# Optimization experiments

Measured on AMD Instinct MI355X. Metric: run time of the kernel, lower is better.

Reference implementation:

```python
import jax, jax.numpy as jnp
import numpy as np

BATCH = 1024
M = 64      # N_v measurements
N = 8192    # N_theta unknowns
STEPS = 3   # N_admm_steps
EPS_DIV = 1e-12


def setup_inputs() -> dict:
    key = jax.random.key(0)
    k = jax.random.split(key, 4)
    return {
        "r_n": jax.random.normal(k[0], (BATCH, 2, N), jnp.float32),
        "y": jax.random.normal(k[1], (BATCH, 2, M), jnp.float32),
        "u_in": jax.random.normal(k[2], (BATCH, 2, M), jnp.float32),
        "A": jax.random.normal(k[3], (2, M, N), jnp.float32) / np.sqrt(N).astype(np.float32),
        "log_rho": jnp.zeros((), jnp.float32),                 # rho = 1.0
        "log_epsilon": jnp.asarray(np.log(0.01), jnp.float32), # epsilon = 0.01
    }


def _cmm(Ar, Ai, v):
    # complex matmul A @ v : v [b,2,N] -> [b,2,M]
    vr, vi = v[:, 0], v[:, 1]
    return jnp.stack([vr @ Ar.T - vi @ Ai.T, vi @ Ar.T + vr @ Ai.T], axis=1)


def _chm(Ar, Ai, v):
    # complex conj-transpose matmul A^H @ v : v [b,2,M] -> [b,2,N]
    vr, vi = v[:, 0], v[:, 1]
    return jnp.stack([vr @ Ar + vi @ Ai, vi @ Ar - vr @ Ai], axis=1)


def reference(r_n, y, u_in, A, log_rho, log_epsilon):
    rho = jnp.exp(log_rho)
    epsilon = jnp.exp(log_epsilon)
    Ar, Ai = A[0], A[1]  # [M, N]

    # SMW system matrix: S = (1/rho) I + A A^H, written as real 2Mx2M block matrix.
    # It is constant across ADMM steps (rho fixed within a forward pass).
    I_M = jnp.eye(M, dtype=A.dtype)
    S_r = I_M / (rho + EPS_DIV) + Ar @ Ar.T + Ai @ Ai.T
    S_i = Ai @ Ar.T - Ar @ Ai.T
    S_block = jnp.block([[S_r, -S_i], [S_i, S_r]])  # [2M, 2M]

    x, z, u = r_n, y, u_in
    for _ in range(STEPS):
        # x-update via SMW: x = b - A^H (S^{-1} A b), b = r_n + rho A^H (z - u)
        b = r_n + rho * _chm(Ar, Ai, z - u)          # [b,2,N]
        Ab = _cmm(Ar, Ai, b)                          # [b,2,M]
        R = jnp.concatenate([Ab[:, 0], Ab[:, 1]], axis=1)  # [b,2M]
        sol = jnp.linalg.solve(S_block, R.T)          # [2M, b]
        T = jnp.stack([sol[:M].T, sol[M:].T], axis=1)  # [b,2,M]
        x = b - _chm(Ar, Ai, T)                       # [b,2,N]
        # enforce_real: zero imaginary part; enforce_positivity: clamp real part
        x = jnp.stack([jnp.maximum(x[:, 0], 0.0), jnp.zeros_like(x[:, 0])], axis=1)
        # z-update: project residual onto complex L2 ball of radius epsilon
        Ax = _cmm(Ar, Ai, x)                          # [b,2,M]
        v = Ax + u - y
        nrm = jnp.sqrt(jnp.sum(v * v, axis=(1, 2), keepdims=True))
        z = y + v * jnp.minimum(1.0, epsilon / (nrm + EPS_DIV))
        # dual update
        u = u + Ax - z
    return x, u
```

## Files before the change

### kernel.cpp

```cpp
#include <hip/hip_runtime.h>

#define B_ 1024
#define M_ 64
#define N_ 8192
#define NSG 16
#define NS3 8

typedef __attribute__((ext_vector_type(8))) short bf16x8;
typedef __attribute__((ext_vector_type(4))) float f32x4;

__device__ inline unsigned short f2b(float f) {
    union { float f; unsigned u; } v; v.f = f;
    unsigned r = v.u + 0x7FFFu + ((v.u >> 16) & 1u);
    return (unsigned short)(r >> 16);
}
__device__ inline unsigned rne2(float lo, float hi) {
    union { float f; unsigned u; } a, b; a.f = lo; b.f = hi;
    unsigned x = (a.u + 0x7FFFu + ((a.u >> 16) & 1u)) >> 16;
    unsigned y = (b.u + 0x7FFFu + ((b.u >> 16) & 1u)) >> 16;
    return x | (y << 16);
}
__device__ inline float b2f(unsigned short s) {
    union { unsigned u; float f; } v; v.u = ((unsigned)s) << 16; return v.f;
}
__device__ inline float rl(float v, int l) {
    return __builtin_bit_cast(float, __builtin_amdgcn_readlane(__builtin_bit_cast(int, v), l));
}

__global__ __launch_bounds__(256) void k_cvt(const float* src, unsigned short* dst) {
    size_t i = ((size_t)blockIdx.x * 256 + threadIdx.x) * 8;
    float4 f0 = *(const float4*)(src + i);
    float4 f1 = *(const float4*)(src + i + 4);
    union { bf16x8 v; unsigned u[4]; } r;
    r.u[0] = rne2(f0.x, f0.y); r.u[1] = rne2(f0.z, f0.w);
    r.u[2] = rne2(f1.x, f1.y); r.u[3] = rne2(f1.z, f1.w);
    *(bf16x8*)(dst + i) = r.v;
}

__global__ __launch_bounds__(256) void k_prep(const float* A, unsigned short* Abf,
                                              unsigned short* WgT, unsigned short* ATb) {
    __shared__ float tile[128][65];
    int n0 = blockIdx.x * 64;
    int t = threadIdx.x;
    int nl = t % 64, r0 = t / 64;
#pragma unroll
    for (int it = 0; it < 32; ++it) {
        int row = r0 + it * 4;
        tile[row][nl] = A[(size_t)row * N_ + n0 + nl];
    }
    __syncthreads();
#pragma unroll
    for (int it = 0; it < 32; ++it) {
        int row = r0 + it * 4;
        float v = tile[row][nl];
        unsigned short bv = f2b(v);
        Abf[(size_t)row * N_ + n0 + nl] = bv;
        if (row < 64) {
            WgT[(size_t)row * 16384 + n0 + nl] = bv;
            WgT[(size_t)(64 + row) * 16384 + 8192 + n0 + nl] = bv;
        } else {
            int m = row - 64;
            WgT[(size_t)m * 16384 + 8192 + n0 + nl] = f2b(-v);
            WgT[(size_t)(64 + m) * 16384 + n0 + nl] = bv;
        }
    }
    int o = t % 128, nn0 = t / 128;
#pragma unroll
    for (int it = 0; it < 32; ++it) {
        int nn = nn0 + it * 2;
        ATb[(size_t)(n0 + nn) * 128 + o] = f2b(tile[o][nn]);
    }
}

__global__ __launch_bounds__(256) void k_Sbuild(const float* A, const float* lr,
                                                float* S, float* AAHT) {
    __shared__ float redS[8];
    int bid = blockIdx.x;
    int i = 0, rem = bid;
    while (rem >= 64 - i) { rem -= 64 - i; ++i; }
    int j = i + rem;
    int t = threadIdx.x;
    const float* Ar = A;
    const float* Ai = A + (size_t)M_ * N_;
    const float* ari = Ar + (size_t)i * N_;
    const float* aii = Ai + (size_t)i * N_;
    const float* arj = Ar + (size_t)j * N_;
    const float* aij = Ai + (size_t)j * N_;
    float aR = 0.f, aI = 0.f;
#pragma unroll
    for (int it = 0; it < 8; ++it) {
        int n = it * 1024 + t * 4;
        float4 xr = *(const float4*)(ari + n);
        float4 xi = *(const float4*)(aii + n);
        float4 br = *(const float4*)(arj + n);
        float4 bi = *(const float4*)(aij + n);
        aR += xr.x * br.x + xi.x * bi.x + xr.y * br.y + xi.y * bi.y
            + xr.z * br.z + xi.z * bi.z + xr.w * br.w + xi.w * bi.w;
        aI += xi.x * br.x - xr.x * bi.x + xi.y * br.y - xr.y * bi.y
            + xi.z * br.z - xr.z * bi.z + xi.w * br.w - xr.w * bi.w;
    }
    for (int off = 32; off > 0; off >>= 1) {
        aR += __shfl_down(aR, off, 64);
        aI += __shfl_down(aI, off, 64);
    }
    int lane = t & 63, w = t >> 6;
    if (lane == 0) { redS[w * 2] = aR; redS[w * 2 + 1] = aI; }
    __syncthreads();
    if (t == 0) {
        float R = redS[0] + redS[2] + redS[4] + redS[6];
        float I = redS[1] + redS[3] + redS[5] + redS[7];
        float inv_rho = 1.0f / (expf(lr[0]) + 1e-12f);
        float diag = (i == j) ? inv_rho : 0.f;
        S[((size_t)i * 64 + j) * 2 + 0] = R + diag;
        S[((size_t)i * 64 + j) * 2 + 1] = I;
        AAHT[((size_t)j * 64 + i) * 2 + 0] = R;
        AAHT[((size_t)j * 64 + i) * 2 + 1] = I;
        if (i != j) {
            S[((size_t)j * 64 + i) * 2 + 0] = R;
            S[((size_t)j * 64 + i) * 2 + 1] = -I;
            AAHT[((size_t)i * 64 + j) * 2 + 0] = R;
            AAHT[((size_t)i * 64 + j) * 2 + 1] = -I;
        }
    }
}

__global__ __launch_bounds__(256, 2) void k_Ginv(const unsigned short* rnb,
                                                 const unsigned short* WgT,
                                                 float* Gpart,
                                                 const float* S, float* Wt) {
    int t = threadIdx.x;
    int lane = t & 63;
    if (blockIdx.x == 0) {
        __shared__ float2 fvs[2][64];
        int g = t >> 6;
        float mx0,my0,mx1,my1,mx2,my2,mx3,my3,mx4,my4,mx5,my5,mx6,my6,mx7,my7;
        float mx8,my8,mx9,my9,mx10,my10,mx11,my11,mx12,my12,mx13,my13,mx14,my14,mx15,my15;
#define GJ_INIT(J) { int c = 4 * (J) + g;                                    \
    float2 v = ((const float2*)S)[(size_t)lane * 64 + c];                    \
    mx##J = v.x; my##J = v.y; }
        GJ_INIT(0) GJ_INIT(1) GJ_INIT(2) GJ_INIT(3) GJ_INIT(4) GJ_INIT(5) GJ_INIT(6) GJ_INIT(7)
        GJ_INIT(8) GJ_INIT(9) GJ_INIT(10) GJ_INIT(11) GJ_INIT(12) GJ_INIT(13) GJ_INIT(14) GJ_INIT(15)
#undef GJ_INIT
        for (int k = 0; k < 64; ++k) {
            const int par = k & 1;
            if (g == (k & 3)) {
                switch (k >> 2) {
                    case 0:  fvs[par][lane] = make_float2(mx0,  my0);  break;
                    case 1:  fvs[par][lane] = make_float2(mx1,  my1);  break;
                    case 2:  fvs[par][lane] = make_float2(mx2,  my2);  break;
                    case 3:  fvs[par][lane] = make_float2(mx3,  my3);  break;
                    case 4:  fvs[par][lane] = make_float2(mx4,  my4);  break;
                    case 5:  fvs[par][lane] = make_float2(mx5,  my5);  break;
                    case 6:  fvs[par][lane] = make_float2(mx6,  my6);  break;
                    case 7:  fvs[par][lane] = make_float2(mx7,  my7);  break;
                    case 8:  fvs[par][lane] = make_float2(mx8,  my8);  break;
                    case 9:  fvs[par][lane] = make_float2(mx9,  my9);  break;
                    case 10: fvs[par][lane] = make_float2(mx10, my10); break;
                    case 11: fvs[par][lane] = make_float2(mx11, my11); break;
                    case 12: fvs[par][lane] = make_float2(mx12, my12); break;
                    case 13: fvs[par][lane] = make_float2(mx13, my13); break;
                    case 14: fvs[par][lane] = make_float2(mx14, my14); break;
                    default: fvs[par][lane] = make_float2(mx15, my15); break;
                }
            }
            __syncthreads();
            float2 f = fvs[par][lane];
            float2 p = fvs[par][k];
            float d = p.x * p.x + p.y * p.y;
            float id = 1.0f / d;
            float pix = p.x * id, piy = -p.y * id;
            bool isk = (lane == k);
            float a   = isk ? 0.f : 1.f;
            float fpx = isk ? -pix : (f.x * pix - f.y * piy);
            float fpy = isk ? -piy : (f.x * piy + f.y * pix);
#define GJ_UP(J) { if (4 * (J) + g == k) { mx##J = -fpx; my##J = -fpy; }     \
    else {                                                                   \
    float sx = rl(mx##J, k), sy = rl(my##J, k);                              \
    float nx = a * mx##J - (fpx * sx - fpy * sy);                            \
    float ny = a * my##J - (fpx * sy + fpy * sx);                            \
    mx##J = nx; my##J = ny; } }
            GJ_UP(0) GJ_UP(1) GJ_UP(2) GJ_UP(3) GJ_UP(4) GJ_UP(5) GJ_UP(6) GJ_UP(7)
            GJ_UP(8) GJ_UP(9) GJ_UP(10) GJ_UP(11) GJ_UP(12) GJ_UP(13) GJ_UP(14) GJ_UP(15)
#undef GJ_UP
        }
#define GJ_OUT(J) { int c = 4 * (J) + g;                                     \
    ((float2*)Wt)[(size_t)c * 64 + lane] = make_float2(mx##J, my##J); }
        GJ_OUT(0) GJ_OUT(1) GJ_OUT(2) GJ_OUT(3) GJ_OUT(4) GJ_OUT(5) GJ_OUT(6) GJ_OUT(7)
        GJ_OUT(8) GJ_OUT(9) GJ_OUT(10) GJ_OUT(11) GJ_OUT(12) GJ_OUT(13) GJ_OUT(14) GJ_OUT(15)
#undef GJ_OUT
        return;
    }
    int bx = blockIdx.x - 1;
    int w = t >> 6;
    int l15 = lane & 15;
    int q8 = (lane >> 4) * 8;
    int split = bx & 15;
    int b0 = (bx >> 4) * 16;
    int k0 = split * 1024;
    f32x4 a00 = {}, a01 = {};
    const unsigned short* x0 = rnb + (size_t)(b0 + l15) * 16384 + k0 + q8;
    const unsigned short* w0 = WgT + (size_t)(w * 32 + l15) * 16384 + k0 + q8;
    const unsigned short* w1 = w0 + (size_t)16 * 16384;
#pragma unroll 8
    for (int ks = 0; ks < 32; ++ks) {
        int kk = ks * 32;
        bf16x8 af0 = *(const bf16x8*)(x0 + kk);
        bf16x8 bf0 = *(const bf16x8*)(w0 + kk);
        bf16x8 bf1 = *(const bf16x8*)(w1 + kk);
        a00 = __builtin_amdgcn_mfma_f32_16x16x32_bf16(af0, bf0, a00, 0, 0, 0);
        a01 = __builtin_amdgcn_mfma_f32_16x16x32_bf16(af0, bf1, a01, 0, 0, 0);
    }
    int row = (lane >> 4) * 4;
    size_t base = (size_t)split * (B_ * 128);
    float* g = Gpart + base + (size_t)(b0 + row) * 128 + w * 32 + l15;
#pragma unroll
    for (int r = 0; r < 4; ++r) {
        g[(size_t)r * 128] = a00[r];
        g[(size_t)r * 128 + 16] = a01[r];
    }
}

__global__ __launch_bounds__(256) void k_small12(const float* Gpart, const float* AAHT,
                                                 const float* Wt, const float* zin,
                                                 const float* uin, const float* lr,
                                                 unsigned short* qb) {
    __shared__ float2 AbS[4][64];
    int t = threadIdx.x;
    int m = t & 63;
    int w = __builtin_amdgcn_readfirstlane(t >> 6);
    int b = blockIdx.x * 4 + w;
    float rho = expf(lr[0]);
    float abR = 0.f, abI = 0.f;
    for (int k = 0; k < 64; ++k) {
        float wr = zin[(b * 2 + 0) * 64 + k] - uin[(b * 2 + 0) * 64 + k];
        float wi = zin[(b * 2 + 1) * 64 + k] - uin[(b * 2 + 1) * 64 + k];
        float2 h = *(const float2*)(AAHT + ((size_t)k * 64 + m) * 2);
        abR += wr * h.x - wi * h.y;
        abI += wi * h.x + wr * h.y;
    }
    float gR = 0.f, gI = 0.f;
#pragma unroll
    for (int s = 0; s < NSG; ++s) {
        gR += Gpart[(size_t)s * 131072 + (size_t)b * 128 + m];
        gI += Gpart[(size_t)s * 131072 + (size_t)b * 128 + 64 + m];
    }
    abR = gR + rho * abR;
    abI = gI + rho * abI;
    AbS[w][m] = make_float2(abR, abI);
    __syncthreads();
    float tR = 0.f, tI = 0.f;
    for (int k = 0; k < 64; ++k) {
        float2 Wv = *(const float2*)(Wt + ((size_t)k * 64 + m) * 2);
        float2 ab = AbS[w][k];
        tR += ab.x * Wv.x - ab.y * Wv.y;
        tI += ab.y * Wv.x + ab.x * Wv.y;
    }
    float wr_m = zin[(b * 2 + 0) * 64 + m] - uin[(b * 2 + 0) * 64 + m];
    float wi_m = zin[(b * 2 + 1) * 64 + m] - uin[(b * 2 + 1) * 64 + m];
    qb[(size_t)b * 128 + m] = f2b(rho * wr_m - tR);
    qb[(size_t)b * 128 + 64 + m] = f2b(rho * wi_m - tI);
}

__global__ __launch_bounds__(256, 3) void k_H23(const unsigned short* qb, const unsigned short* ATb,
                                                const unsigned short* rnb, const unsigned short* Abf,
                                                float* out, float* Axpart, int last) {
    __shared__ __align__(16) char lds_buf[4 * 8448];
    int t = threadIdx.x;
    int lane = t & 63;
    int w = t >> 6;
    int l15 = lane & 15;
    int q8 = (lane >> 4) * 8;
    int row = (lane >> 4) * 4;
    int slab = blockIdx.x;
    int b0 = blockIdx.y * 16;
    int n0 = slab * 1024 + w * 256;
    short* xs = (short*)(lds_buf + w * 8448);
    float* rs = (float*)(lds_buf + w * 8448);

    bf16x8 a[4];
    const unsigned short* qrow = qb + (size_t)(b0 + l15) * 128 + q8;
#pragma unroll
    for (int ks = 0; ks < 4; ++ks) a[ks] = *(const bf16x8*)(qrow + ks * 32);
#pragma unroll 2
    for (int nt = 0; nt < 16; ++nt) {
        f32x4 acc = {};
        const unsigned short* bbase = ATb + (size_t)(n0 + nt * 16 + l15) * 128 + q8;
#pragma unroll
        for (int ks = 0; ks < 4; ++ks) {
            bf16x8 bf = *(const bf16x8*)(bbase + ks * 32);
            acc = __builtin_amdgcn_mfma_f32_16x16x32_bf16(a[ks], bf, acc, 0, 0, 0);
        }
        int ncol = n0 + nt * 16 + l15;
        int nloc = nt * 16 + l15;
#pragma unroll
        for (int r = 0; r < 4; ++r) {
            size_t ridx = (size_t)(b0 + row + r) * 16384 + ncol;
            float v = fmaxf(acc[r] + b2f(rnb[ridx]), 0.f);
            if (last) out[ridx] = v;
            xs[(row + r) * 264 + nloc] = (short)f2b(v);
        }
    }
    f32x4 acc8[8] = {};
#pragma unroll
    for (int ks = 0; ks < 8; ++ks) {
        bf16x8 xf = *(const bf16x8*)(xs + l15 * 264 + ks * 32 + q8);
#pragma unroll
        for (int ot = 0; ot < 8; ++ot) {
            const unsigned short* bp = Abf + (size_t)(ot * 16 + l15) * 8192 + n0 + ks * 32 + q8;
            acc8[ot] = __builtin_amdgcn_mfma_f32_16x16x32_bf16(xf, *(const bf16x8*)bp, acc8[ot], 0, 0, 0);
        }
    }
    __syncthreads();
#pragma unroll
    for (int ot = 0; ot < 8; ++ot)
#pragma unroll
        for (int r = 0; r < 4; ++r)
            rs[(row + r) * 132 + ot * 16 + l15] = acc8[ot][r];
    __syncthreads();
#pragma unroll
    for (int e = t; e < 2048; e += 256) {
        int b = e >> 7, o = e & 127;
        float sAx = 0.f;
#pragma unroll
        for (int ww = 0; ww < 4; ++ww)
            sAx += ((const float*)(lds_buf + ww * 8448))[b * 132 + o];
        Axpart[(size_t)slab * 131072 + (size_t)(b0 + b) * 128 + o] = sAx;
    }
    if (last) {
        float4 z4 = make_float4(0.f, 0.f, 0.f, 0.f);
        for (int e = t; e < 4096; e += 256) {
            int bb = e >> 8, nq = e & 255;
            *(float4*)(out + ((size_t)(b0 + bb) * 2 + 1) * N_ + slab * 1024 + nq * 4) = z4;
        }
    }
}

__global__ __launch_bounds__(128) void k_small3(const float* Axpart, const float* uin,
                                                const float* y, const float* le,
                                                float* z, float* u, float* uout, int last) {
    __shared__ float red[2];
    int b = blockIdx.x, t = threadIdx.x;
    size_t idx = (size_t)b * 128 + t;
    float ax = 0.f;
#pragma unroll
    for (int s = 0; s < NS3; ++s) ax += Axpart[(size_t)s * 131072 + idx];
    float uo = uin[idx], yv = y[idx];
    float v = ax + uo - yv;
    float sq = v * v;
    for (int off = 32; off > 0; off >>= 1) sq += __shfl_down(sq, off, 64);
    if ((t & 63) == 0) red[t >> 6] = sq;
    __syncthreads();
    float tot = red[0] + red[1];
    float eps = expf(le[0]);
    float scale = fminf(1.f, eps / (sqrtf(tot) + 1e-12f));
    float zv = yv + v * scale;
    float un = uo + ax - zv;
    z[idx] = zv;
    u[idx] = un;
    if (last) uout[idx] = un;
}

extern "C" void kernel_launch(void* const* d_in, const int* in_sizes, int n_in,
                              void* d_out, int out_size, void* d_ws, size_t ws_size,
                              hipStream_t stream) {
    const float* rn  = (const float*)d_in[0];
    const float* y   = (const float*)d_in[1];
    const float* uin = (const float*)d_in[2];
    const float* A   = (const float*)d_in[3];
    const float* lr  = (const float*)d_in[4];
    const float* le  = (const float*)d_in[5];

    float* out = (float*)d_out;
    float* ws  = (float*)d_ws;

    float* Gpart  = ws;
    float* Axpart = Gpart + (size_t)NSG * 131072;
    float* S      = Axpart + (size_t)NS3 * 131072;
    float* AAHT   = S + 8192;
    float* Wt     = AAHT + 8192;
    float* z      = Wt + 8192;
    float* u      = z + 131072;
    unsigned short* qb  = (unsigned short*)(u + 131072);
    unsigned short* rnb = qb + 131072;
    unsigned short* WgT = rnb + (size_t)B_ * 16384;
    unsigned short* Abf = WgT + 2097152;
    unsigned short* ATb = Abf + 1048576;
    float* uout = out + (size_t)B_ * 2 * N_;

    k_prep<<<128, 256, 0, stream>>>(A, Abf, WgT, ATb);
    k_cvt<<<8192, 256, 0, stream>>>(rn, rnb);
    k_Sbuild<<<2080, 256, 0, stream>>>(A, lr, S, AAHT);
    k_Ginv<<<1025, 256, 0, stream>>>(rnb, WgT, Gpart, S, Wt);

    for (int step = 0; step < 3; ++step) {
        const float* zp = (step == 0) ? y   : z;
        const float* up = (step == 0) ? uin : u;
        int last = (step == 2) ? 1 : 0;
        k_small12<<<256, 256, 0, stream>>>(Gpart, AAHT, Wt, zp, up, lr, qb);
        k_H23<<<dim3(NS3, 64), 256, 0, stream>>>(qb, ATb, rnb, Abf, out, Axpart, last);
        k_small3<<<B_, 128, 0, stream>>>(Axpart, up, y, le, z, u, uout, last);
    }
}
```

Baseline: 378.7 us.

## Block the in-place Gauss-Jordan inversion into 16-column panels to cut barriers

The 64x64 complex matrix inversion in block 0 switches from a cyclic column distribution with one __syncthreads per pivot to a blocked layout. Each wave owns 16 contiguous columns, factors its panel locally with lane shuffles, publishes the transform through shared memory, and the other waves apply a rank-16 trailing update. This cuts the barrier count from 64 to 4 and turns per-pivot updates into denser FMA chains. The cost is that the other waves idle while one wave factors its panel, and this inversion runs in a single block alongside the GEMM blocks.

Measured after the change: 420.8 us. 1.11x slower.

```diff
diff --git a/kernel.cpp b/kernel.cpp
--- a/kernel.cpp
+++ b/kernel.cpp
@@ -131,59 +131,72 @@
     int t = threadIdx.x;
     int lane = t & 63;
     if (blockIdx.x == 0) {
-        __shared__ float2 fvs[2][64];
+        __shared__ float2 Tp[2][16][64];
         int g = t >> 6;
         float mx0,my0,mx1,my1,mx2,my2,mx3,my3,mx4,my4,mx5,my5,mx6,my6,mx7,my7;
         float mx8,my8,mx9,my9,mx10,my10,mx11,my11,mx12,my12,mx13,my13,mx14,my14,mx15,my15;
-#define GJ_INIT(J) { int c = 4 * (J) + g;                                    \
+#define GJ_INIT(J) { int c = 16 * g + (J);                                   \
     float2 v = ((const float2*)S)[(size_t)lane * 64 + c];                    \
     mx##J = v.x; my##J = v.y; }
         GJ_INIT(0) GJ_INIT(1) GJ_INIT(2) GJ_INIT(3) GJ_INIT(4) GJ_INIT(5) GJ_INIT(6) GJ_INIT(7)
         GJ_INIT(8) GJ_INIT(9) GJ_INIT(10) GJ_INIT(11) GJ_INIT(12) GJ_INIT(13) GJ_INIT(14) GJ_INIT(15)
 #undef GJ_INIT
-        for (int k = 0; k < 64; ++k) {
-            const int par = k & 1;
-            if (g == (k & 3)) {
-                switch (k >> 2) {
-                    case 0:  fvs[par][lane] = make_float2(mx0,  my0);  break;
-                    case 1:  fvs[par][lane] = make_float2(mx1,  my1);  break;
-                    case 2:  fvs[par][lane] = make_float2(mx2,  my2);  break;
-                    case 3:  fvs[par][lane] = make_float2(mx3,  my3);  break;
-                    case 4:  fvs[par][lane] = make_float2(mx4,  my4);  break;
-                    case 5:  fvs[par][lane] = make_float2(mx5,  my5);  break;
-                    case 6:  fvs[par][lane] = make_float2(mx6,  my6);  break;
-                    case 7:  fvs[par][lane] = make_float2(mx7,  my7);  break;
-                    case 8:  fvs[par][lane] = make_float2(mx8,  my8);  break;
-                    case 9:  fvs[par][lane] = make_float2(mx9,  my9);  break;
-                    case 10: fvs[par][lane] = make_float2(mx10, my10); break;
-                    case 11: fvs[par][lane] = make_float2(mx11, my11); break;
-                    case 12: fvs[par][lane] = make_float2(mx12, my12); break;
-                    case 13: fvs[par][lane] = make_float2(mx13, my13); break;
-                    case 14: fvs[par][lane] = make_float2(mx14, my14); break;
-                    default: fvs[par][lane] = make_float2(mx15, my15); break;
-                }
-            }
-            __syncthreads();
-            float2 f = fvs[par][lane];
-            float2 p = fvs[par][k];
-            float d = p.x * p.x + p.y * p.y;
-            float id = 1.0f / d;
-            float pix = p.x * id, piy = -p.y * id;
-            bool isk = (lane == k);
-            float a   = isk ? 0.f : 1.f;
-            float fpx = isk ? -pix : (f.x * pix - f.y * piy);
-            float fpy = isk ? -piy : (f.x * piy + f.y * pix);
-#define GJ_UP(J) { if (4 * (J) + g == k) { mx##J = -fpx; my##J = -fpy; }     \
-    else {                                                                   \
+
+#define FUP(J, j) if ((J) != (j)) {                                          \
     float sx = rl(mx##J, k), sy = rl(my##J, k);                              \
     float nx = a * mx##J - (fpx * sx - fpy * sy);                            \
     float ny = a * my##J - (fpx * sy + fpy * sx);                            \
-    mx##J = nx; my##J = ny; } }
-            GJ_UP(0) GJ_UP(1) GJ_UP(2) GJ_UP(3) GJ_UP(4) GJ_UP(5) GJ_UP(6) GJ_UP(7)
-            GJ_UP(8) GJ_UP(9) GJ_UP(10) GJ_UP(11) GJ_UP(12) GJ_UP(13) GJ_UP(14) GJ_UP(15)
-#undef GJ_UP
-        }
-#define GJ_OUT(J) { int c = 4 * (J) + g;                                     \
+    mx##J = nx; my##J = ny; }
+#define FACT_STEP(j) {                                                       \
+    int k = 16 * p + (j);                                                    \
+    float px = rl(mx##j, k), py = rl(my##j, k);                              \
+    float d = px * px + py * py;                                             \
+    float id = 1.0f / d;                                                     \
+    float pix = px * id, piy = -py * id;                                     \
+    bool isk = (lane == k);                                                  \
+    float a   = isk ? 0.f : 1.f;                                             \
+    float fpx = isk ? -pix : (mx##j * pix - my##j * piy);                    \
+    float fpy = isk ? -piy : (mx##j * piy + my##j * pix);                    \
+    FUP(0, j) FUP(1, j) FUP(2, j) FUP(3, j) FUP(4, j) FUP(5, j) FUP(6, j) FUP(7, j) \
+    FUP(8, j) FUP(9, j) FUP(10, j) FUP(11, j) FUP(12, j) FUP(13, j) FUP(14, j) FUP(15, j) \
+    mx##j = -fpx; my##j = -fpy; }
+
+        for (int p = 0; p < 4; ++p) {
+            const int buf = p & 1;
+            if (g == p) {
+                FACT_STEP(0)  FACT_STEP(1)  FACT_STEP(2)  FACT_STEP(3)
+                FACT_STEP(4)  FACT_STEP(5)  FACT_STEP(6)  FACT_STEP(7)
+                FACT_STEP(8)  FACT_STEP(9)  FACT_STEP(10) FACT_STEP(11)
+                FACT_STEP(12) FACT_STEP(13) FACT_STEP(14) FACT_STEP(15)
+#define GJ_PUB(J) Tp[buf][J][lane] = make_float2(mx##J, my##J);
+                GJ_PUB(0) GJ_PUB(1) GJ_PUB(2) GJ_PUB(3) GJ_PUB(4) GJ_PUB(5) GJ_PUB(6) GJ_PUB(7)
+                GJ_PUB(8) GJ_PUB(9) GJ_PUB(10) GJ_PUB(11) GJ_PUB(12) GJ_PUB(13) GJ_PUB(14) GJ_PUB(15)
+#undef GJ_PUB
+            }
+            __syncthreads();
+            if (g != p) {
+#define TL(j) float tx##j = Tp[buf][j][lane].x, ty##j = Tp[buf][j][lane].y;
+                TL(0) TL(1) TL(2) TL(3) TL(4) TL(5) TL(6) TL(7)
+                TL(8) TL(9) TL(10) TL(11) TL(12) TL(13) TL(14) TL(15)
+#undef TL
+                float msk = ((lane >> 4) == p) ? 0.f : 1.f;
+#define TFMA(j, J) { float sx = rl(mx##J, 16 * p + (j)), sy = rl(my##J, 16 * p + (j)); \
+    ax += tx##j * sx - ty##j * sy; ay += tx##j * sy + ty##j * sx; }
+#define TRAIL_COL(J) { float ax = msk * mx##J, ay = msk * my##J;             \
+    TFMA(0, J) TFMA(1, J) TFMA(2, J) TFMA(3, J) TFMA(4, J) TFMA(5, J) TFMA(6, J) TFMA(7, J) \
+    TFMA(8, J) TFMA(9, J) TFMA(10, J) TFMA(11, J) TFMA(12, J) TFMA(13, J) TFMA(14, J) TFMA(15, J) \
+    mx##J = ax; my##J = ay; }
+                TRAIL_COL(0)  TRAIL_COL(1)  TRAIL_COL(2)  TRAIL_COL(3)
+                TRAIL_COL(4)  TRAIL_COL(5)  TRAIL_COL(6)  TRAIL_COL(7)
+                TRAIL_COL(8)  TRAIL_COL(9)  TRAIL_COL(10) TRAIL_COL(11)
+                TRAIL_COL(12) TRAIL_COL(13) TRAIL_COL(14) TRAIL_COL(15)
+#undef TRAIL_COL
+#undef TFMA
+            }
+        }
+#undef FACT_STEP
+#undef FUP
+#define GJ_OUT(J) { int c = 16 * g + (J);                                    \
     ((float2*)Wt)[(size_t)c * 64 + lane] = make_float2(mx##J, my##J); }
         GJ_OUT(0) GJ_OUT(1) GJ_OUT(2) GJ_OUT(3) GJ_OUT(4) GJ_OUT(5) GJ_OUT(6) GJ_OUT(7)
         GJ_OUT(8) GJ_OUT(9) GJ_OUT(10) GJ_OUT(11) GJ_OUT(12) GJ_OUT(13) GJ_OUT(14) GJ_OUT(15)
```
